# Performance work log

Measured on AMD Instinct MI355X. Metric: run time of the kernel, lower is better.

The kernel has to match this reference:

```python
import jax, jax.numpy as jnp
import numpy as np

N_EL, N_NB, DIM = 8192, 24, 256
CUTOFF = 5.0
F0, F1 = 32, 16
N_ENV = 8
N_FEAT = 4  # [dist, dx, dy, dz]


def setup_inputs() -> dict:
    key = jax.random.key(0)
    ks = jax.random.split(key, 24)
    d = {}
    d['elec'] = jax.random.normal(ks[0], (N_EL, DIM), jnp.float32)
    d['msg'] = jax.random.normal(ks[1], (N_EL, DIM), jnp.float32)
    # positions inside a box of half the cutoff so pairs are within range
    d['r'] = jax.random.uniform(ks[2], (N_EL, 3), jnp.float32) * (0.5 * CUTOFF)
    d['r_nb'] = jax.random.uniform(ks[3], (N_EL, N_NB, 3), jnp.float32) * (0.5 * CUTOFF)
    d['s'] = jax.random.randint(ks[4], (N_EL,), 0, 2, jnp.int32)
    d['s_nb'] = jax.random.randint(ks[5], (N_EL, N_NB), 0, 2, jnp.int32)
    d['hinit_nb'] = jax.random.normal(ks[6], (N_EL, N_NB, DIM), jnp.float32)
    # parameters
    def lecun(k, shape):
        fan_in = shape[0]
        return jax.random.normal(k, shape, jnp.float32) / np.float32(np.sqrt(fan_in))
    d['W_in'] = lecun(ks[7], (DIM, DIM)); d['b_in'] = jnp.zeros((DIM,), jnp.float32)
    d['ee_scales'] = jax.random.uniform(ks[8], (N_ENV,), jnp.float32, 0.5, CUTOFF)
    d['ee_kernel'] = lecun(ks[9], (N_FEAT, F0))
    d['ee_bias'] = 2.0 * jax.random.normal(ks[10], (F0,), jnp.float32)
    d['Wf'] = lecun(ks[11], (F0 + N_ENV, F1)); d['bf'] = jnp.zeros((F1,), jnp.float32)
    d['Wsame'] = lecun(ks[12], (F1, DIM))
    d['Wdiff'] = lecun(ks[13], (F1, DIM))
    d['W1'] = lecun(ks[14], (DIM, DIM)); d['b1'] = jnp.zeros((DIM,), jnp.float32)
    d['W2'] = lecun(ks[15], (DIM, DIM)); d['b2'] = jnp.zeros((DIM,), jnp.float32)
    d['W3'] = lecun(ks[16], (DIM, DIM)); d['b3'] = jnp.zeros((DIM,), jnp.float32)
    d['scale'] = jnp.float32(1.0)  # FixedScalingFactor (identity at init)
    return d


def _forward(elec, msg, r, r_nb, s, s_nb, hinit_nb,
             W_in, b_in, ee_scales, ee_kernel, ee_bias, Wf, bf,
             Wsame, Wdiff, W1, b1, W2, b2, W3, b3, scale):
    silu = jax.nn.silu
    elec1 = silu(elec @ W_in + b_in)                       # [N, D]
    # get_diff_features: [dist, dx, dy, dz]
    diff = r_nb - r[:, None, :]                             # [N, K, 3]
    dist = jnp.sqrt(jnp.sum(diff * diff, -1) + 1e-12)       # [N, K]
    feats = jnp.concatenate([dist[..., None], diff], -1)    # [N, K, 4]
    spin_mask = s[:, None] == s_nb                          # [N, K]
    # PairwiseFilter: MLP on diff-features + radial envelopes, smooth cutoff
    env = jnp.exp(-jnp.square(dist[..., None] / ee_scales)) # [N, K, E]
    h = silu(feats @ ee_kernel + ee_bias)                   # [N, K, F0]
    h = jnp.concatenate([h, env], -1)                       # [N, K, F0+E]
    x = dist / CUTOFF
    cut = jnp.where(dist < CUTOFF, jnp.square(1.0 - x) * (1.0 + 2.0 * x), 0.0)
    beta = (h @ Wf + bf) * cut[..., None]                   # [N, K, F1]
    gamma = jnp.where(spin_mask[..., None], beta @ Wsame, beta @ Wdiff)  # [N, K, D]
    hinit_msg = jnp.einsum('nid,nid->nd', silu(elec1[:, None] + hinit_nb), gamma)
    out = silu(elec1 @ W1 + b1 + hinit_msg)
    out = silu(out @ W2 + b2 + msg)
    out = silu(out @ W3 + b3)
    return (out + elec1) * scale


def reference(elec, msg, r, r_nb, s, s_nb, hinit_nb,
              W_in, b_in, ee_scales, ee_kernel, ee_bias, Wf, bf,
              Wsame, Wdiff, W1, b1, W2, b2, W3, b3, scale):
    return _forward(elec, msg, r, r_nb, s, s_nb, hinit_nb,
                    W_in, b_in, ee_scales, ee_kernel, ee_bias, Wf, bf,
                    Wsame, Wdiff, W1, b1, W2, b2, W3, b3, scale)
```

## Files before the change

### kernel.cpp

```cpp
#include <hip/hip_runtime.h>

#define DIM 256
#define PDIM 260
#define PD2  264
#define SBPITCH 20
#define SGPITCH 40
#define NNB 24
#define NEL 8192
#define ROWS 16
#define NT 512
#define CUTOFF 5.0f

typedef unsigned int u32;
typedef unsigned short u16;
typedef __attribute__((ext_vector_type(8))) short bf16x8;
typedef __attribute__((ext_vector_type(4))) float f32x4;

__device__ __forceinline__ u16 f2b(float f){
  union{float f;u32 i;}v; v.f=f;
  u32 r = v.i + 0x7fffu + ((v.i>>16)&1u);
  return (u16)(r>>16);
}
__device__ __forceinline__ float b2f(u16 u){
  union{u32 i;float f;}v; v.i = ((u32)u)<<16; return v.f;
}
__device__ __forceinline__ float fast_silu(float x){
  float e = __builtin_amdgcn_exp2f(-1.44269504088896340f * x);
  return x * __builtin_amdgcn_rcpf(1.0f + e);
}

__global__ __launch_bounds__(256)
void wprep(const float* __restrict__ W0, const float* __restrict__ W1,
           const float* __restrict__ W2, const float* __restrict__ W3,
           const float* __restrict__ Wsame, const float* __restrict__ Wdiff,
           u16* __restrict__ ws){
  if (blockIdx.x < 1024){
    const int mat = blockIdx.x >> 8;
    const int n   = blockIdx.x & 255;
    const int k   = threadIdx.x;
    const float* W = (mat==0)?W0:(mat==1)?W1:(mat==2)?W2:W3;
    ws[(mat<<16) + (n<<8) + k] = f2b(W[(k<<8) + n]);
  } else {
    const int n = threadIdx.x;
    u16* dst = ws + 4*65536 + n*32;
    #pragma unroll
    for (int kk = 0; kk < 16; kk++){
      dst[kk]    = f2b(Wsame[kk*DIM + n]);
      dst[16+kk] = f2b(Wdiff[kk*DIM + n]);
    }
  }
}

template<int MODE, int ABF16>
__device__ __forceinline__ void gemm_mfma(
    const void* A, u16* sE1b, float* sR1,
    const u16* __restrict__ Wt, const float* __restrict__ bias,
    const float* __restrict__ extraGbl, float* __restrict__ outGbl,
    float scl, int n0, int t)
{
  const int lane = t & 63;
  const int ln   = lane & 15;
  const int quad = lane >> 4;
  const int nt0  = (t >> 6) << 1;
  f32x4 acc0 = {0.f,0.f,0.f,0.f};
  f32x4 acc1 = {0.f,0.f,0.f,0.f};
  const u16* bp0 = Wt + (nt0*16 + ln)*DIM;
  const u16* bp1 = bp0 + 16*DIM;
  #pragma unroll
  for (int ks = 0; ks < 8; ks++){
    const int k0 = ks*32 + quad*8;
    bf16x8 af;
    if (ABF16){
      af = *(const bf16x8*)((const u16*)A + ln*PD2 + k0);
    } else {
      const float* arow = (const float*)A + ln*PDIM;
      float4 a01 = *(const float4*)(arow + k0);
      float4 a23 = *(const float4*)(arow + k0 + 4);
      af[0]=(short)f2b(a01.x); af[1]=(short)f2b(a01.y);
      af[2]=(short)f2b(a01.z); af[3]=(short)f2b(a01.w);
      af[4]=(short)f2b(a23.x); af[5]=(short)f2b(a23.y);
      af[6]=(short)f2b(a23.z); af[7]=(short)f2b(a23.w);
    }
    bf16x8 b0 = *(const bf16x8*)(bp0 + k0);
    bf16x8 b1 = *(const bf16x8*)(bp1 + k0);
    acc0 = __builtin_amdgcn_mfma_f32_16x16x32_bf16(af, b0, acc0, 0, 0, 0);
    acc1 = __builtin_amdgcn_mfma_f32_16x16x32_bf16(af, b1, acc1, 0, 0, 0);
  }
  if (MODE == 2) __syncthreads();
  #pragma unroll
  for (int r = 0; r < 4; r++){
    const int m = quad*4 + r;
    #pragma unroll
    for (int tt = 0; tt < 2; tt++){
      const int n = (nt0+tt)*16 + ln;
      float v = (tt ? acc1[r] : acc0[r]) + bias[n];
      if (MODE == 1) v += sR1[m*PDIM + n];
      if (MODE == 2) v += extraGbl[(size_t)(n0+m)*DIM + n];
      v = fast_silu(v);
      if (MODE == 0)      sE1b[m*PD2 + n] = f2b(v);
      else if (MODE == 3) outGbl[(size_t)(n0+m)*DIM + n] = (v + b2f(sE1b[m*PD2 + n])) * scl;
      else                sR1[m*PDIM + n] = v;
    }
  }
}

__global__ __launch_bounds__(NT, 4)
void fused_moon_kernel(
    const float* __restrict__ elec, const float* __restrict__ msg,
    const float* __restrict__ rpos, const float* __restrict__ rnb,
    const int* __restrict__ s,    const int* __restrict__ snb,
    const float* __restrict__ hinit,
    const float* __restrict__ bin,
    const float* __restrict__ eesc, const float* __restrict__ eek,
    const float* __restrict__ eeb,  const float* __restrict__ Wf,
    const float* __restrict__ bfb,
    const float* __restrict__ b1, const float* __restrict__ b2,
    const float* __restrict__ b3,
    const float* __restrict__ scalep,
    const u16* __restrict__ Wt,
    float* __restrict__ out)
{
  __shared__ float sR1[ROWS*PDIM];
  __shared__ u16   sE1b[ROWS*PD2];
  __shared__ u16   sBC[NNB*16*SBPITCH];
  __shared__ int   sMask[ROWS*NNB];
  __shared__ float sG[8*16*SGPITCH];
  const int t  = threadIdx.x;
  const int n0 = blockIdx.x * ROWS;

  {
    const float4* ep = (const float4*)elec;
    #pragma unroll
    for (int h = 0; h < 2; h++){
      const int idx = t + h*NT;
      float4 v = ep[(size_t)n0*64 + idx];
      *(float4*)&sR1[(idx>>6)*PDIM + (idx&63)*4] = v;
    }
  }
  __syncthreads();

  gemm_mfma<0,0>(sR1, sE1b, sR1, Wt, bin, nullptr, nullptr, 0.f, n0, t);

  if (t < ROWS*NNB) {
    const int rr = t / NNB;
    const int k  = t - rr*NNB;
    const int n  = n0 + rr;
    const float* rp  = rpos + n*3;
    const float* rnp = rnb + (n*NNB + k)*3;
    float dx = rnp[0] - rp[0];
    float dy = rnp[1] - rp[1];
    float dz = rnp[2] - rp[2];
    float dist = sqrtf(dx*dx + dy*dy + dz*dz + 1e-12f);
    float feats[4] = {dist, dx, dy, dz};
    float h[32];
    #pragma unroll
    for (int f4 = 0; f4 < 8; f4++){
      float4 a4 = *(const float4*)&eeb[4*f4];
      float av[4] = {a4.x, a4.y, a4.z, a4.w};
      #pragma unroll
      for (int i = 0; i < 4; i++){
        float4 kv = *(const float4*)&eek[i*32 + 4*f4];
        av[0]+=feats[i]*kv.x; av[1]+=feats[i]*kv.y; av[2]+=feats[i]*kv.z; av[3]+=feats[i]*kv.w;
      }
      h[4*f4+0]=fast_silu(av[0]); h[4*f4+1]=fast_silu(av[1]);
      h[4*f4+2]=fast_silu(av[2]); h[4*f4+3]=fast_silu(av[3]);
    }
    float env[8];
    #pragma unroll
    for (int e = 0; e < 8; e++){
      float q = dist * __builtin_amdgcn_rcpf(eesc[e]);
      env[e] = __builtin_amdgcn_exp2f(-1.44269504088896340f * q * q);
    }
    float xx = dist * (1.0f/CUTOFF);
    float cut = (dist < CUTOFF) ? (1.0f-xx)*(1.0f-xx)*(1.0f+2.0f*xx) : 0.0f;
    u16* rowp = &sBC[(k*16 + rr)*SBPITCH];
    #pragma unroll
    for (int j4 = 0; j4 < 4; j4++){
      float4 a4 = *(const float4*)&bfb[4*j4];
      float av[4] = {a4.x, a4.y, a4.z, a4.w};
      #pragma unroll
      for (int f = 0; f < 40; f++){
        float val = (f < 32) ? h[f] : env[f-32];
        float4 wv = *(const float4*)&Wf[f*16 + 4*j4];
        av[0]+=val*wv.x; av[1]+=val*wv.y; av[2]+=val*wv.z; av[3]+=val*wv.w;
      }
      ushort4 bv;
      bv.x = f2b(av[0]*cut); bv.y = f2b(av[1]*cut);
      bv.z = f2b(av[2]*cut); bv.w = f2b(av[3]*cut);
      *(ushort4*)(rowp + 4*j4) = bv;
    }
    sMask[rr*NNB + k] = (s[n] == snb[n*NNB + k]) ? 1 : 0;
  }
  __syncthreads();

  {
    const int lane = t & 63;
    const int ln   = lane & 15;
    const int quad = lane >> 4;
    const int w    = t >> 6;
    const int C0   = w << 5;
    const u16* Wcat = Wt + 4*65536;
    bf16x8 bs0 = *(const bf16x8*)(Wcat + (C0 + ln)*32 + quad*8);
    bf16x8 bs1 = *(const bf16x8*)(Wcat + (C0 + 16 + ln)*32 + quad*8);
    float* sGw = &sG[w*16*SGPITCH];

    const int rowA = lane >> 3;
    const int rowB = rowA + 8;
    const int c4   = (lane & 7) << 2;
    float e1A[4], e1B[4];
    {
      ushort4 ea = *(const ushort4*)&sE1b[rowA*PD2 + C0 + c4];
      ushort4 eb = *(const ushort4*)&sE1b[rowB*PD2 + C0 + c4];
      e1A[0]=b2f(ea.x); e1A[1]=b2f(ea.y); e1A[2]=b2f(ea.z); e1A[3]=b2f(ea.w);
      e1B[0]=b2f(eb.x); e1B[1]=b2f(eb.y); e1B[2]=b2f(eb.z); e1B[3]=b2f(eb.w);
    }
    const float* hpA = hinit + (size_t)(n0 + rowA)*NNB*DIM + C0 + c4;
    const float* hpB = hpA + (size_t)8*NNB*DIM;
    float hmA[4] = {0.f,0.f,0.f,0.f};
    float hmB[4] = {0.f,0.f,0.f,0.f};
    float4 hA = *(const float4*)(hpA);
    float4 hB = *(const float4*)(hpB);
    for (int k = 0; k < NNB; k++){
      const int kn = (k+1 < NNB) ? (k+1) : (NNB-1);
      float4 hA2 = *(const float4*)(hpA + kn*DIM);
      float4 hB2 = *(const float4*)(hpB + kn*DIM);
      bf16x8 b8 = *(const bf16x8*)(&sBC[(k*16 + ln)*SBPITCH + (quad&1)*8]);
      const int mm = sMask[ln*NNB + k];
      const u16 km = (u16)((((quad>>1) ^ mm) != 0) ? 0xFFFFu : 0u);
      bf16x8 af;
      #pragma unroll
      for (int j = 0; j < 8; j++) af[j] = (short)(((u16)af[j], (u16)b8[j]) & km);
      f32x4 z = {0.f,0.f,0.f,0.f};
      f32x4 g0 = __builtin_amdgcn_mfma_f32_16x16x32_bf16(af, bs0, z, 0, 0, 0);
      f32x4 g1 = __builtin_amdgcn_mfma_f32_16x16x32_bf16(af, bs1, z, 0, 0, 0);
      __builtin_amdgcn_wave_barrier();
      #pragma unroll
      for (int r = 0; r < 4; r++){
        sGw[(quad*4+r)*SGPITCH + ln]      = g0[r];
        sGw[(quad*4+r)*SGPITCH + 16 + ln] = g1[r];
      }
      __builtin_amdgcn_wave_barrier();
      float4 gA = *(const float4*)&sGw[rowA*SGPITCH + c4];
      float4 gB = *(const float4*)&sGw[rowB*SGPITCH + c4];
      __builtin_amdgcn_wave_barrier();
      hmA[0] += fast_silu(e1A[0]+hA.x)*gA.x; hmA[1] += fast_silu(e1A[1]+hA.y)*gA.y;
      hmA[2] += fast_silu(e1A[2]+hA.z)*gA.z; hmA[3] += fast_silu(e1A[3]+hA.w)*gA.w;
      hmB[0] += fast_silu(e1B[0]+hB.x)*gB.x; hmB[1] += fast_silu(e1B[1]+hB.y)*gB.y;
      hmB[2] += fast_silu(e1B[2]+hB.z)*gB.z; hmB[3] += fast_silu(e1B[3]+hB.w)*gB.w;
      hA = hA2; hB = hB2;
    }
    *(float4*)&sR1[rowA*PDIM + C0 + c4] = make_float4(hmA[0],hmA[1],hmA[2],hmA[3]);
    *(float4*)&sR1[rowB*PDIM + C0 + c4] = make_float4(hmB[0],hmB[1],hmB[2],hmB[3]);
  }
  __syncthreads();

  const float scl = scalep[0];

  gemm_mfma<1,1>(sE1b, sE1b, sR1, Wt + (1<<16), b1, nullptr, nullptr, 0.f, n0, t);
  __syncthreads();
  gemm_mfma<2,0>(sR1, sE1b, sR1, Wt + (2<<16), b2, msg, nullptr, 0.f, n0, t);
  __syncthreads();
  gemm_mfma<3,0>(sR1, sE1b, sR1, Wt + (3<<16), b3, nullptr, out, scl, n0, t);
}

extern "C" void kernel_launch(void* const* d_in, const int* in_sizes, int n_in,
                              void* d_out, int out_size, void* d_ws, size_t ws_size,
                              hipStream_t stream) {
  (void)in_sizes; (void)n_in; (void)ws_size; (void)out_size;
  const float* elec  = (const float*)d_in[0];
  const float* msg   = (const float*)d_in[1];
  const float* rpos  = (const float*)d_in[2];
  const float* rnb   = (const float*)d_in[3];
  const int*   s     = (const int*)d_in[4];
  const int*   snb   = (const int*)d_in[5];
  const float* hinit = (const float*)d_in[6];
  const float* Win   = (const float*)d_in[7];
  const float* bin   = (const float*)d_in[8];
  const float* eesc  = (const float*)d_in[9];
  const float* eek   = (const float*)d_in[10];
  const float* eeb   = (const float*)d_in[11];
  const float* Wf    = (const float*)d_in[12];
  const float* bfb   = (const float*)d_in[13];
  const float* Wsame = (const float*)d_in[14];
  const float* Wdiff = (const float*)d_in[15];
  const float* W1    = (const float*)d_in[16];
  const float* b1    = (const float*)d_in[17];
  const float* W2    = (const float*)d_in[18];
  const float* b2    = (const float*)d_in[19];
  const float* W3    = (const float*)d_in[20];
  const float* b3    = (const float*)d_in[21];
  const float* scl   = (const float*)d_in[22];
  float* outp        = (float*)d_out;
  u16*   wt          = (u16*)d_ws;

  wprep<<<dim3(1025), dim3(256), 0, stream>>>(Win, W1, W2, W3, Wsame, Wdiff, wt);
  fused_moon_kernel<<<dim3(NEL/ROWS), dim3(NT), 0, stream>>>(
      elec, msg, rpos, rnb, s, snb, hinit,
      bin, eesc, eek, eeb, Wf, bfb,
      b1, b2, b3, scl, wt, outp);
}
```

Baseline: 368.1 us.

## Swap MFMA operands to consume gamma in registers and deepen hinit prefetch

The MFMA operands are swapped so each lane's output fragment lines up with the hinit columns it owns. This removes the per-neighbor LDS round trip through sG and its wave barriers. The spin mask is packed into a per-row bitmask built with shared atomicOr, and hinit loads are prefetched three neighbors ahead instead of one. The cost is higher register pressure from the deeper prefetch, and the hinit global access pattern changes: each lane now reads rows strided by ln with 16-column gaps, which may hurt coalescing.

```diff
diff --git a/kernel.cpp b/kernel.cpp
--- a/kernel.cpp
+++ b/kernel.cpp
@@ -4,7 +4,6 @@
 #define PDIM 260
 #define PD2  264
 #define SBPITCH 20
-#define SGPITCH 40
 #define NNB 24
 #define NEL 8192
 #define ROWS 16
@@ -123,11 +122,11 @@
   __shared__ float sR1[ROWS*PDIM];
   __shared__ u16   sE1b[ROWS*PD2];
   __shared__ u16   sBC[NNB*16*SBPITCH];
-  __shared__ int   sMask[ROWS*NNB];
-  __shared__ float sG[8*16*SGPITCH];
+  __shared__ u32   sMaskB[ROWS];
   const int t  = threadIdx.x;
   const int n0 = blockIdx.x * ROWS;
 
+  if (t < ROWS) sMaskB[t] = 0u;
   {
     const float4* ep = (const float4*)elec;
     #pragma unroll
@@ -189,7 +188,7 @@
       bv.z = f2b(av[2]*cut); bv.w = f2b(av[3]*cut);
       *(ushort4*)(rowp + 4*j4) = bv;
     }
-    sMask[rr*NNB + k] = (s[n] == snb[n*NNB + k]) ? 1 : 0;
+    if (s[n] == snb[n*NNB + k]) atomicOr(&sMaskB[rr], 1u << k);
   }
   __syncthreads();
 
@@ -199,58 +198,53 @@
     const int quad = lane >> 4;
     const int w    = t >> 6;
     const int C0   = w << 5;
+    const int nA   = C0 + (quad << 2);
     const u16* Wcat = Wt + 4*65536;
     bf16x8 bs0 = *(const bf16x8*)(Wcat + (C0 + ln)*32 + quad*8);
     bf16x8 bs1 = *(const bf16x8*)(Wcat + (C0 + 16 + ln)*32 + quad*8);
-    float* sGw = &sG[w*16*SGPITCH];
-
-    const int rowA = lane >> 3;
-    const int rowB = rowA + 8;
-    const int c4   = (lane & 7) << 2;
+
     float e1A[4], e1B[4];
     {
-      ushort4 ea = *(const ushort4*)&sE1b[rowA*PD2 + C0 + c4];
-      ushort4 eb = *(const ushort4*)&sE1b[rowB*PD2 + C0 + c4];
+      ushort4 ea = *(const ushort4*)&sE1b[ln*PD2 + nA];
+      ushort4 eb = *(const ushort4*)&sE1b[ln*PD2 + nA + 16];
       e1A[0]=b2f(ea.x); e1A[1]=b2f(ea.y); e1A[2]=b2f(ea.z); e1A[3]=b2f(ea.w);
       e1B[0]=b2f(eb.x); e1B[1]=b2f(eb.y); e1B[2]=b2f(eb.z); e1B[3]=b2f(eb.w);
     }
-    const float* hpA = hinit + (size_t)(n0 + rowA)*NNB*DIM + C0 + c4;
-    const float* hpB = hpA + (size_t)8*NNB*DIM;
+    const u32 mb = sMaskB[ln];
+    const float* hp = hinit + (size_t)(n0 + ln)*NNB*DIM + nA;
+    float4 hA0 = *(const float4*)(hp + 0*DIM);
+    float4 hB0 = *(const float4*)(hp + 0*DIM + 16);
+    float4 hA1 = *(const float4*)(hp + 1*DIM);
+    float4 hB1 = *(const float4*)(hp + 1*DIM + 16);
+    float4 hA2 = *(const float4*)(hp + 2*DIM);
+    float4 hB2 = *(const float4*)(hp + 2*DIM + 16);
     float hmA[4] = {0.f,0.f,0.f,0.f};
     float hmB[4] = {0.f,0.f,0.f,0.f};
-    float4 hA = *(const float4*)(hpA);
-    float4 hB = *(const float4*)(hpB);
     for (int k = 0; k < NNB; k++){
-      const int kn = (k+1 < NNB) ? (k+1) : (NNB-1);
-      float4 hA2 = *(const float4*)(hpA + kn*DIM);
-      float4 hB2 = *(const float4*)(hpB + kn*DIM);
+      const int kp = (k+3 < NNB) ? (k+3) : (NNB-1);
+      float4 hA3 = *(const float4*)(hp + kp*DIM);
+      float4 hB3 = *(const float4*)(hp + kp*DIM + 16);
       bf16x8 b8 = *(const bf16x8*)(&sBC[(k*16 + ln)*SBPITCH + (quad&1)*8]);
-      const int mm = sMask[ln*NNB + k];
-      const u16 km = (u16)((((quad>>1) ^ mm) != 0) ? 0xFFFFu : 0u);
+      const u16 km = (u16)((((u32)(quad>>1) ^ ((mb>>k)&1u)) != 0u) ? 0xFFFFu : 0u);
       bf16x8 af;
       #pragma unroll
-      for (int j = 0; j < 8; j++) af[j] = (short)(((u16)af[j], (u16)b8[j]) & km);
+      for (int j = 0; j < 8; j++) af[j] = (short)((u16)b8[j] & km);
       f32x4 z = {0.f,0.f,0.f,0.f};
-      f32x4 g0 = __builtin_amdgcn_mfma_f32_16x16x32_bf16(af, bs0, z, 0, 0, 0);
-      f32x4 g1 = __builtin_amdgcn_mfma_f32_16x16x32_bf16(af, bs1, z, 0, 0, 0);
-      __builtin_amdgcn_wave_barrier();
-      #pragma unroll
-      for (int r = 0; r < 4; r++){
-        sGw[(quad*4+r)*SGPITCH + ln]      = g0[r];
-        sGw[(quad*4+r)*SGPITCH + 16 + ln] = g1[r];
-      }
-      __builtin_amdgcn_wave_barrier();
-      float4 gA = *(const float4*)&sGw[rowA*SGPITCH + c4];
-      float4 gB = *(const float4*)&sGw[rowB*SGPITCH + c4];
-      __builtin_amdgcn_wave_barrier();
-      hmA[0] += fast_silu(e1A[0]+hA.x)*gA.x; hmA[1] += fast_silu(e1A[1]+hA.y)*gA.y;
-      hmA[2] += fast_silu(e1A[2]+hA.z)*gA.z; hmA[3] += fast_silu(e1A[3]+hA.w)*gA.w;
-      hmB[0] += fast_silu(e1B[0]+hB.x)*gB.x; hmB[1] += fast_silu(e1B[1]+hB.y)*gB.y;
-      hmB[2] += fast_silu(e1B[2]+hB.z)*gB.z; hmB[3] += fast_silu(e1B[3]+hB.w)*gB.w;
-      hA = hA2; hB = hB2;
-    }
-    *(float4*)&sR1[rowA*PDIM + C0 + c4] = make_float4(hmA[0],hmA[1],hmA[2],hmA[3]);
-    *(float4*)&sR1[rowB*PDIM + C0 + c4] = make_float4(hmB[0],hmB[1],hmB[2],hmB[3]);
+      f32x4 g0 = __builtin_amdgcn_mfma_f32_16x16x32_bf16(bs0, af, z, 0, 0, 0);
+      f32x4 g1 = __builtin_amdgcn_mfma_f32_16x16x32_bf16(bs1, af, z, 0, 0, 0);
+      hmA[0] += fast_silu(e1A[0]+hA0.x)*g0[0];
+      hmA[1] += fast_silu(e1A[1]+hA0.y)*g0[1];
+      hmA[2] += fast_silu(e1A[2]+hA0.z)*g0[2];
+      hmA[3] += fast_silu(e1A[3]+hA0.w)*g0[3];
+      hmB[0] += fast_silu(e1B[0]+hB0.x)*g1[0];
+      hmB[1] += fast_silu(e1B[1]+hB0.y)*g1[1];
+      hmB[2] += fast_silu(e1B[2]+hB0.z)*g1[2];
+      hmB[3] += fast_silu(e1B[3]+hB0.w)*g1[3];
+      hA0=hA1; hA1=hA2; hA2=hA3;
+      hB0=hB1; hB1=hB2; hB2=hB3;
+    }
+    *(float4*)&sR1[ln*PDIM + nA]      = make_float4(hmA[0],hmA[1],hmA[2],hmA[3]);
+    *(float4*)&sR1[ln*PDIM + nA + 16] = make_float4(hmB[0],hmB[1],hmB[2],hmB[3]);
   }
   __syncthreads();
 
```

New measurement: 368.7 us. About the same (+0.2%).
